# Performance work log

Measured on AMD Instinct MI355X. Metric: run time of the kernel, lower is better.

Reference implementation:

```python
import jax, jax.numpy as jnp
import numpy as np

NEG = -1000000000.0


def setup_inputs() -> dict:
    key = jax.random.key(0)
    ks = jax.random.split(key, 10)
    B, C, D, E, V, G = 512, 200, 512, 256, 8192, 2048  # batch, max_ctx, decoder, embed, vocab, 4*D
    batched_context = jax.random.normal(ks[0], (B, C, D), dtype=jnp.float32)
    counts = jax.random.randint(ks[1], (B,), 1, C + 1, dtype=jnp.int32)
    emb_table = jax.random.normal(ks[2], (V, E), dtype=jnp.float32) * 0.02
    emb_table = emb_table.at[0].set(0.0)  # padding_idx = 0
    W_attn = jax.random.normal(ks[3], (D, D), dtype=jnp.float32) * 0.02
    W_ih = jax.random.normal(ks[4], (G, E + D), dtype=jnp.float32) * 0.02
    b_ih = jax.random.normal(ks[5], (G,), dtype=jnp.float32) * 0.02
    W_hh = jax.random.normal(ks[6], (G, D), dtype=jnp.float32) * 0.02
    b_hh = jax.random.normal(ks[7], (G,), dtype=jnp.float32) * 0.02
    W_proj = jax.random.normal(ks[8], (V, D), dtype=jnp.float32) * 0.02
    b_proj = jax.random.normal(ks[9], (V,), dtype=jnp.float32) * 0.02
    return {
        "batched_context": batched_context, "counts": counts, "output_length": 16,
        "emb_table": emb_table, "W_attn": W_attn, "W_ih": W_ih, "b_ih": b_ih,
        "W_hh": W_hh, "b_hh": b_hh, "W_proj": W_proj, "b_proj": b_proj,
    }


def _decode(batched_context, counts, output_length, emb_table, W_attn, W_ih, b_ih, W_hh, b_hh, W_proj, b_proj):
    B, C, D = batched_context.shape
    V = emb_table.shape[0]
    sos_token = 1
    valid = (jnp.arange(C)[None, :] < counts[:, None])  # [B, C]
    attn_mask = jnp.where(valid, 0.0, NEG).astype(batched_context.dtype)
    # initial state: mean over valid contexts per label
    ctx_masked = batched_context * valid[:, :, None].astype(batched_context.dtype)
    init_state = ctx_masked.sum(axis=1) / counts[:, None].astype(batched_context.dtype)  # [B, D]

    def step(carry, _):
        h, c, tok = carry
        emb = emb_table[tok]  # [B, E]
        # Luong attention on last-layer hidden
        q = h @ W_attn.T  # [B, D]
        score = jnp.einsum("bcd,bd->bc", batched_context, q) + attn_mask
        w = jax.nn.softmax(score, axis=1)  # [B, C]
        context = jnp.einsum("bc,bcd->bd", w, batched_context)  # [B, D]
        x = jnp.concatenate([emb, context], axis=1)  # [B, E+D]
        gates = x @ W_ih.T + b_ih + h @ W_hh.T + b_hh  # [B, 4D]
        i, f, g, o = jnp.split(gates, 4, axis=1)  # PyTorch gate order i,f,g,o
        c_new = jax.nn.sigmoid(f) * c + jax.nn.sigmoid(i) * jnp.tanh(g)
        h_new = jax.nn.sigmoid(o) * jnp.tanh(c_new)
        logits = h_new @ W_proj.T + b_proj  # [B, V]
        tok_new = jnp.argmax(logits, axis=-1)
        return (h_new, c_new, tok_new), logits

    tok0 = jnp.full((B,), sos_token, dtype=jnp.int32)
    _, outs = jax.lax.scan(step, (init_state, init_state, tok0), None, length=output_length - 1)
    zeros0 = jnp.zeros((1, B, V), dtype=batched_context.dtype)  # output[0] stays zero
    return jnp.concatenate([zeros0, outs], axis=0)  # [L, B, V]


def reference(batched_context, counts, output_length, emb_table, W_attn, W_ih, b_ih, W_hh, b_hh, W_proj, b_proj):
    return _decode(batched_context, counts, output_length, emb_table, W_attn, W_ih, b_ih, W_hh, b_hh, W_proj, b_proj)
```

## Files before the change

kernel.cpp:

```cpp
#include <hip/hip_runtime.h>
#include <math.h>

#define B_ 512
#define C_ 200
#define D_ 512
#define E_ 256
#define V_ 8192
#define G_ 2048
#define L_ 16

typedef __attribute__((ext_vector_type(8))) short short8;
typedef __attribute__((ext_vector_type(4))) float f32x4;

__device__ __forceinline__ float sigm(float x) { return 1.0f / (1.0f + expf(-x)); }

__device__ __forceinline__ unsigned short bf16_rn(float x) {
    unsigned int u = __float_as_uint(x);
    return (unsigned short)((u + 0x7FFFu + ((u >> 16) & 1u)) >> 16);
}
__device__ __forceinline__ float bf16f(unsigned short h) {
    return __uint_as_float(((unsigned int)h) << 16);
}


__global__ __launch_bounds__(256) void k_setup(const float* __restrict__ W_proj,
                                               const float* __restrict__ emb,
                                               const float* __restrict__ W_ih,
                                               const float* __restrict__ W_hh,
                                               const float* __restrict__ W_attn,
                                               const float* __restrict__ ctx,
                                               const int* __restrict__ counts,
                                               unsigned short* __restrict__ WpC_hi,
                                               unsigned short* __restrict__ WpC_lo,
                                               unsigned short* __restrict__ Eb_hi,
                                               unsigned short* __restrict__ Eb_lo,
                                               unsigned short* __restrict__ WgC_hi,
                                               unsigned short* __restrict__ WgC_lo,
                                               unsigned short* __restrict__ WaC_hi,
                                               unsigned short* __restrict__ WaC_lo,
                                               unsigned short* __restrict__ h_hi,
                                               unsigned short* __restrict__ h_lo,
                                               float* __restrict__ c,
                                               int* __restrict__ tok) {
    int bb = blockIdx.x;
    int t = threadIdx.x;
    if (bb < 2048) {
        int i = bb * 256 + t;
        int n = i >> 6;
        int koff = (i & 63) * 8;
        float4 v0 = *(const float4*)&W_proj[(size_t)n * 512 + koff];
        float4 v1 = *(const float4*)&W_proj[(size_t)n * 512 + koff + 4];
        float vv[8] = {v0.x, v0.y, v0.z, v0.w, v1.x, v1.y, v1.z, v1.w};
        short8 h8, l8;
#pragma unroll
        for (int e = 0; e < 8; ++e) {
            unsigned short hh = bf16_rn(vv[e]);
            h8[e] = (short)hh;
            l8[e] = (short)bf16_rn(vv[e] - bf16f(hh));
        }
        int nt = n >> 4, srow = n & 15, ktile = koff >> 5, oct = (koff >> 3) & 3;
        size_t off = (((size_t)nt * 16 + ktile) * 64 + (srow + (oct << 4))) * 8;
        *(short8*)&WpC_hi[off] = h8;
        *(short8*)&WpC_lo[off] = l8;
    } else if (bb < 4096) {
        int i = (bb - 2048) * 256 + t;
        float4 v = ((const float4*)emb)[i];
        ushort4 h, l;
        h.x = bf16_rn(v.x); l.x = bf16_rn(v.x - bf16f(h.x));
        h.y = bf16_rn(v.y); l.y = bf16_rn(v.y - bf16f(h.y));
        h.z = bf16_rn(v.z); l.z = bf16_rn(v.z - bf16f(h.z));
        h.w = bf16_rn(v.w); l.w = bf16_rn(v.w - bf16f(h.w));
        ((ushort4*)Eb_hi)[i] = h;
        ((ushort4*)Eb_lo)[i] = l;
    } else if (bb < 5376) {
        int i = (bb - 4096) * 256 + t;
        if (i < 327680) {
            int r = i / 160;
            int koff = (i - r * 160) * 8;
            int go = ((r & 3) << 9) + (r >> 2);
            float4 v0, v1;
            if (koff < 768) {
                v0 = *(const float4*)&W_ih[(size_t)go * 768 + koff];
                v1 = *(const float4*)&W_ih[(size_t)go * 768 + koff + 4];
            } else {
                v0 = *(const float4*)&W_hh[(size_t)go * 512 + (koff - 768)];
                v1 = *(const float4*)&W_hh[(size_t)go * 512 + (koff - 768) + 4];
            }
            float vv[8] = {v0.x, v0.y, v0.z, v0.w, v1.x, v1.y, v1.z, v1.w};
            short8 h8, l8;
#pragma unroll
            for (int e = 0; e < 8; ++e) {
                unsigned short hh = bf16_rn(vv[e]);
                h8[e] = (short)hh;
                l8[e] = (short)bf16_rn(vv[e] - bf16f(hh));
            }
            int nt = r >> 4, srow = r & 15, ktile = koff >> 5, oct = (koff >> 3) & 3;
            size_t off = (((size_t)nt * 40 + ktile) * 64 + (srow + (oct << 4))) * 8;
            *(short8*)&WgC_hi[off] = h8;
            *(short8*)&WgC_lo[off] = l8;
        }
    } else if (bb < 5504) {
        int i = (bb - 5376) * 256 + t;
        int n = i >> 6;
        int koff = (i & 63) * 8;
        float4 v0 = *(const float4*)&W_attn[(size_t)n * 512 + koff];
        float4 v1 = *(const float4*)&W_attn[(size_t)n * 512 + koff + 4];
        float vv[8] = {v0.x, v0.y, v0.z, v0.w, v1.x, v1.y, v1.z, v1.w};
        short8 h8, l8;
#pragma unroll
        for (int e = 0; e < 8; ++e) {
            unsigned short hh = bf16_rn(vv[e]);
            h8[e] = (short)hh;
            l8[e] = (short)bf16_rn(vv[e] - bf16f(hh));
        }
        int nt = n >> 4, srow = n & 15, ktile = koff >> 5, oct = (koff >> 3) & 3;
        size_t off = (((size_t)nt * 16 + ktile) * 64 + (srow + (oct << 4))) * 8;
        *(short8*)&WaC_hi[off] = h8;
        *(short8*)&WaC_lo[off] = l8;
    } else {
        int b = bb - 5504;
        int cnt = counts[b];
        const float* base = ctx + (size_t)b * C_ * D_;
        float s0 = 0.f, s1 = 0.f;
        for (int cc = 0; cc < cnt; ++cc) {
            s0 += base[(size_t)cc * D_ + t];
            s1 += base[(size_t)cc * D_ + t + 256];
        }
        float inv = 1.0f / (float)cnt;
        float v0 = s0 * inv, v1 = s1 * inv;
        c[b * D_ + t] = v0;       c[b * D_ + t + 256] = v1;
        unsigned short p0 = bf16_rn(v0), p1 = bf16_rn(v1);
        h_hi[b * D_ + t] = p0;    h_hi[b * D_ + t + 256] = p1;
        h_lo[b * D_ + t] = bf16_rn(v0 - bf16f(p0));
        h_lo[b * D_ + t + 256] = bf16_rn(v1 - bf16f(p1));
        if (t == 0) tok[b] = 1;
    }
}

template<int PART>
__device__ __forceinline__ void gemm_body(int nb, int mb,
                                          const unsigned short* __restrict__ Ah,
                                          const unsigned short* __restrict__ Al,
                                          const unsigned short* __restrict__ BhC,
                                          const unsigned short* __restrict__ BlC,
                                          const float* __restrict__ bias,
                                          float* __restrict__ C, int ldc,
                                          float* __restrict__ pvO,
                                          int* __restrict__ piO,
                                          short* As,
                                          float (*pvS)[2], int (*piS)[2]) {
    int t = threadIdx.x;
    int l = t & 63;
    int w = t >> 6;
    int m0 = mb * 64;
    int n0 = nb * 128;
    int srow = l & 15;
    int koct = 8 * (l >> 4);
    int pl = w & 1;
    int mtA = w >> 1;
    int wm = w >> 1, wn = w & 1;
    const unsigned short* Apl = pl ? Al : Ah;
    const unsigned short* ApA = Apl + (size_t)(m0 + mtA * 16 + srow) * 512 + koct;
    const unsigned short* ApB = ApA + 32 * 512;
    int ntbase = nb * 8 + wn * 4;
    const unsigned short* Bh0 = BhC + ((size_t)ntbase * 16) * 512 + l * 8;
    const unsigned short* Bl0 = BlC + ((size_t)ntbase * 16) * 512 + l * 8;

    short8 rA0 = *(const short8*)(ApA);
    short8 rA1 = *(const short8*)(ApB);

    f32x4 z = {0.f, 0.f, 0.f, 0.f};
    f32x4 acc[2][4];
#pragma unroll
    for (int i = 0; i < 2; ++i)
#pragma unroll
        for (int j = 0; j < 4; ++j) acc[i][j] = z;

    for (int kt = 0; kt < 16; ++kt) {
        short8 bh[4], bl[4];
#pragma unroll
        for (int j = 0; j < 4; ++j) {
            bh[j] = *(const short8*)(Bh0 + ((size_t)j * 16 + kt) * 512);
            bl[j] = *(const short8*)(Bl0 + ((size_t)j * 16 + kt) * 512);
        }
        __syncthreads();
        *(short8*)&As[(w)*512 + l * 8] = rA0;
        *(short8*)&As[(w + 4) * 512 + l * 8] = rA1;
        __syncthreads();
        if (kt + 1 < 16) {
            int ke = kt * 32;
            rA0 = *(const short8*)(ApA + ke + 32);
            rA1 = *(const short8*)(ApB + ke + 32);
        }
        short8 ah[2], al2[2];
#pragma unroll
        for (int i = 0; i < 2; ++i) {
            ah[i] = *(short8*)&As[((wm * 2 + i) * 2 + 0) * 512 + l * 8];
            al2[i] = *(short8*)&As[((wm * 2 + i) * 2 + 1) * 512 + l * 8];
        }
#pragma unroll
        for (int i = 0; i < 2; ++i)
#pragma unroll
            for (int j = 0; j < 4; ++j) {
                acc[i][j] = __builtin_amdgcn_mfma_f32_16x16x32_bf16(ah[i], bh[j], acc[i][j], 0, 0, 0);
                acc[i][j] = __builtin_amdgcn_mfma_f32_16x16x32_bf16(ah[i], bl[j], acc[i][j], 0, 0, 0);
                acc[i][j] = __builtin_amdgcn_mfma_f32_16x16x32_bf16(al2[i], bh[j], acc[i][j], 0, 0, 0);
            }
    }
    int r0 = (l >> 4) * 4;
    int cl = l & 15;
    if (PART) {
        float bj_[4];
#pragma unroll
        for (int j = 0; j < 4; ++j) bj_[j] = bias[n0 + wn * 64 + j * 16 + cl];
#pragma unroll
        for (int i = 0; i < 2; ++i) {
#pragma unroll
            for (int r = 0; r < 4; ++r) {
                int row = m0 + wm * 32 + i * 16 + r0 + r;
                float bv = -INFINITY;
                int bidx = 0x7fffffff;
#pragma unroll
                for (int j = 0; j < 4; ++j) {
                    int col = n0 + wn * 64 + j * 16 + cl;
                    float v = acc[i][j][r] + bj_[j];
                    C[(size_t)row * ldc + col] = v;
                    if (v > bv) { bv = v; bidx = col; }
                }
#pragma unroll
                for (int off = 1; off < 16; off <<= 1) {
                    float ov = __shfl_xor(bv, off);
                    int oi = __shfl_xor(bidx, off);
                    if (ov > bv || (ov == bv && oi < bidx)) { bv = ov; bidx = oi; }
                }
                if (cl == 0) {
                    pvS[wm * 32 + i * 16 + r0 + r][wn] = bv;
                    piS[wm * 32 + i * 16 + r0 + r][wn] = bidx;
                }
            }
        }
        __syncthreads();
        if (t < 64) {
            float v0 = pvS[t][0], v1 = pvS[t][1];
            int i0 = piS[t][0], i1 = piS[t][1];
            bool take1 = (v1 > v0);
            pvO[(size_t)(m0 + t) * 64 + nb] = take1 ? v1 : v0;
            piO[(size_t)(m0 + t) * 64 + nb] = take1 ? i1 : i0;
        }
    } else {
#pragma unroll
        for (int i = 0; i < 2; ++i)
#pragma unroll
            for (int j = 0; j < 4; ++j) {
                int col = n0 + wn * 64 + j * 16 + cl;
                int rowb = m0 + wm * 32 + i * 16 + r0;
#pragma unroll
                for (int r = 0; r < 4; ++r)
                    C[(size_t)(rowb + r) * ldc + col] = acc[i][j][r];
            }
    }
}

__global__ __launch_bounds__(256, 2) void k_mega(const unsigned short* __restrict__ Ah,
                                                 const unsigned short* __restrict__ Al,
                                                 const unsigned short* __restrict__ WpCh,
                                                 const unsigned short* __restrict__ WpCl,
                                                 const float* __restrict__ bias,
                                                 float* __restrict__ Cl_,
                                                 float* __restrict__ pvO,
                                                 int* __restrict__ piO,
                                                 const unsigned short* __restrict__ WaCh,
                                                 const unsigned short* __restrict__ WaCl,
                                                 float* __restrict__ qbuf) {
    __shared__ short As[8 * 512];
    __shared__ float pvS[64][2];
    __shared__ int piS[64][2];
    int bb = blockIdx.x;
    if (bb < 512) {
        int xcd = bb & 7, lid = bb >> 3;
        int nb = xcd * 8 + (lid & 7);
        int mb = lid >> 3;
        gemm_body<1>(nb, mb, Ah, Al, WpCh, WpCl, bias, Cl_, V_, pvO, piO,
                     As, pvS, piS);
    } else {
        int idx = bb - 512;
        int nb = idx & 3, mb = idx >> 2;
        gemm_body<0>(nb, mb, Ah, Al, WaCh, WaCl, nullptr, qbuf, D_, nullptr, nullptr,
                     As, pvS, piS);
    }
}

__global__ __launch_bounds__(256, 2) void k_qproj(const unsigned short* __restrict__ Ah,
                                                  const unsigned short* __restrict__ Al,
                                                  const unsigned short* __restrict__ WaCh,
                                                  const unsigned short* __restrict__ WaCl,
                                                  float* __restrict__ qbuf) {
    __shared__ short As[8 * 512];
    __shared__ float pvS[64][2];
    __shared__ int piS[64][2];
    int nb = blockIdx.x & 3, mb = blockIdx.x >> 2;
    gemm_body<0>(nb, mb, Ah, Al, WaCh, WaCl, nullptr, qbuf, D_, nullptr, nullptr,
                 As, pvS, piS);
}

__global__ __launch_bounds__(256) void k_attn(const float* __restrict__ ctx,
                                              const int* __restrict__ counts,
                                              const float* __restrict__ q,
                                              unsigned short* __restrict__ cv_hi,
                                              unsigned short* __restrict__ cv_lo) {
    __shared__ float accw[4][512];
    __shared__ float mw_s[4], sw_s[4];
    int b = blockIdx.x;
    int t = threadIdx.x;
    int lane = t & 63;
    int wv = t >> 6;
    int cnt = counts[b];
    const float* cb = ctx + (size_t)b * C_ * D_;

    float4 q0 = *(const float4*)&q[(size_t)b * D_ + lane * 4];
    float4 q1 = *(const float4*)&q[(size_t)b * D_ + lane * 4 + 256];

    float m_w = -INFINITY, s_w = 0.f;
    float4 a0 = make_float4(0.f, 0.f, 0.f, 0.f);
    float4 a1 = make_float4(0.f, 0.f, 0.f, 0.f);

#define ATT_DOT(x0, x1) (x0.x * q0.x + x0.y * q0.y + x0.z * q0.z + x0.w * q0.w + \
                         x1.x * q1.x + x1.y * q1.y + x1.z * q1.z + x1.w * q1.w)
#define ATT_UPD(s, x0, x1)                                                     \
    {                                                                          \
        float e;                                                               \
        if (s > m_w) {                                                         \
            float sc = expf(m_w - s);                                          \
            s_w = s_w * sc + 1.f;                                              \
            a0.x *= sc; a0.y *= sc; a0.z *= sc; a0.w *= sc;                    \
            a1.x *= sc; a1.y *= sc; a1.z *= sc; a1.w *= sc;                    \
            m_w = s; e = 1.f;                                                  \
        } else {                                                               \
            e = expf(s - m_w);                                                 \
            s_w += e;                                                          \
        }                                                                      \
        a0.x += e * x0.x; a0.y += e * x0.y; a0.z += e * x0.z; a0.w += e * x0.w;\
        a1.x += e * x1.x; a1.y += e * x1.y; a1.z += e * x1.z; a1.w += e * x1.w;\
    }

    int cc = wv;
    for (; cc + 4 < cnt; cc += 8) {
        const float* rA = cb + (size_t)cc * D_;
        const float* rB = cb + (size_t)(cc + 4) * D_;
        float4 xa0 = *(const float4*)&rA[lane * 4];
        float4 xa1 = *(const float4*)&rA[lane * 4 + 256];
        float4 xb0 = *(const float4*)&rB[lane * 4];
        float4 xb1 = *(const float4*)&rB[lane * 4 + 256];
        float sa = ATT_DOT(xa0, xa1);
        float sb = ATT_DOT(xb0, xb1);
#pragma unroll
        for (int off = 32; off; off >>= 1) {
            sa += __shfl_xor(sa, off);
            sb += __shfl_xor(sb, off);
        }
        ATT_UPD(sa, xa0, xa1);
        ATT_UPD(sb, xb0, xb1);
    }
    if (cc < cnt) {
        const float* rA = cb + (size_t)cc * D_;
        float4 xa0 = *(const float4*)&rA[lane * 4];
        float4 xa1 = *(const float4*)&rA[lane * 4 + 256];
        float sa = ATT_DOT(xa0, xa1);
#pragma unroll
        for (int off = 32; off; off >>= 1) sa += __shfl_xor(sa, off);
        ATT_UPD(sa, xa0, xa1);
    }

    accw[wv][lane * 4 + 0] = a0.x; accw[wv][lane * 4 + 1] = a0.y;
    accw[wv][lane * 4 + 2] = a0.z; accw[wv][lane * 4 + 3] = a0.w;
    accw[wv][256 + lane * 4 + 0] = a1.x; accw[wv][256 + lane * 4 + 1] = a1.y;
    accw[wv][256 + lane * 4 + 2] = a1.z; accw[wv][256 + lane * 4 + 3] = a1.w;
    if (lane == 0) { mw_s[wv] = m_w; sw_s[wv] = s_w; }
    __syncthreads();

    float m_g = fmaxf(fmaxf(mw_s[0], mw_s[1]), fmaxf(mw_s[2], mw_s[3]));
    float e0 = expf(mw_s[0] - m_g), e1 = expf(mw_s[1] - m_g);
    float e2 = expf(mw_s[2] - m_g), e3 = expf(mw_s[3] - m_g);
    float inv = 1.0f / (sw_s[0] * e0 + sw_s[1] * e1 + sw_s[2] * e2 + sw_s[3] * e3);
    float v0 = (accw[0][t] * e0 + accw[1][t] * e1 + accw[2][t] * e2 + accw[3][t] * e3) * inv;
    float v1 = (accw[0][t + 256] * e0 + accw[1][t + 256] * e1 +
                accw[2][t + 256] * e2 + accw[3][t + 256] * e3) * inv;
    unsigned short p0 = bf16_rn(v0), p1 = bf16_rn(v1);
    cv_hi[(size_t)b * D_ + t] = p0;
    cv_hi[(size_t)b * D_ + t + 256] = p1;
    cv_lo[(size_t)b * D_ + t] = bf16_rn(v0 - bf16f(p0));
    cv_lo[(size_t)b * D_ + t + 256] = bf16_rn(v1 - bf16f(p1));
}

template<int RED>
__global__ __launch_bounds__(256, 2) void k_gatesm(const int* __restrict__ tok,
                                                   const float* __restrict__ pvO,
                                                   const int* __restrict__ piO,
                                                   const unsigned short* __restrict__ Eh,
                                                   const unsigned short* __restrict__ El,
                                                   const unsigned short* __restrict__ Ch,
                                                   const unsigned short* __restrict__ Cl,
                                                   const unsigned short* __restrict__ Hh,
                                                   const unsigned short* __restrict__ Hl,
                                                   const unsigned short* __restrict__ WgCh,
                                                   const unsigned short* __restrict__ WgCl,
                                                   const float* __restrict__ b_ih,
                                                   const float* __restrict__ b_hh,
                                                   float* __restrict__ cbuf,
                                                   unsigned short* __restrict__ Hoh,
                                                   unsigned short* __restrict__ Hol) {
    __shared__ short As[8 * 512];
    __shared__ int toks[64];
    int bid = blockIdx.x;
    int t = threadIdx.x;
    int l = t & 63;
    int w = t >> 6;
    int xcd = bid & 7, lid = bid >> 3;
    int nb = xcd * 8 + (lid & 7);
    int mb = lid >> 3;
    int m0 = mb * 64;
    int n0 = nb * 32;
    int srow = l & 15;
    int koct = 8 * (l >> 4);
    int pl = w & 1;
    int mtA = w >> 1;
    int locA = mtA * 16 + srow;
    int rowA = m0 + locA;
    int rowB = rowA + 32;

    if (RED) {
        int ri = t >> 2, qq = t & 3;
        const float* pv = pvO + (size_t)(m0 + ri) * 64 + qq * 16;
        const int* pi = piO + (size_t)(m0 + ri) * 64 + qq * 16;
        float bv = -INFINITY;
        int bix = 0x7fffffff;
#pragma unroll
        for (int j = 0; j < 16; ++j) {
            float v = pv[j];
            int ii = pi[j];
            if (v > bv || (v == bv && ii < bix)) { bv = v; bix = ii; }
        }
#pragma unroll
        for (int off = 1; off < 4; off <<= 1) {
            float ov = __shfl_xor(bv, off);
            int oi = __shfl_xor(bix, off);
            if (ov > bv || (ov == bv && oi < bix)) { bv = ov; bix = oi; }
        }
        if (qq == 0) toks[ri] = bix;
        __syncthreads();
    }

    int tokA = RED ? toks[locA] : tok[rowA];
    int tokB = RED ? toks[locA + 32] : tok[rowB];

    const unsigned short* Ep = pl ? El : Eh;
    const unsigned short* Cp = pl ? Cl : Ch;
    const unsigned short* Hp = pl ? Hl : Hh;
    int wm = w >> 1, wn = w & 1;
    int ntg = nb * 2 + wn;
    const unsigned short* Bh0 = WgCh + ((size_t)ntg * 40) * 512 + l * 8;
    const unsigned short* Bl0 = WgCl + ((size_t)ntg * 40) * 512 + l * 8;

    f32x4 z = {0.f, 0.f, 0.f, 0.f};
    f32x4 acc[2];
    acc[0] = z; acc[1] = z;

    short8 rA0, rA1;

#define GATES_LOADA(dst, row, tk, kk)                                          \
    {                                                                          \
        int kx = (kk);                                                         \
        if (kx < 256)      dst = *(const short8*)&Ep[(size_t)(tk)*256 + kx];   \
        else if (kx < 768) dst = *(const short8*)&Cp[(size_t)(row)*512 + (kx - 256)]; \
        else               dst = *(const short8*)&Hp[(size_t)(row)*512 + (kx - 768)]; \
    }

    GATES_LOADA(rA0, rowA, tokA, koct);
    GATES_LOADA(rA1, rowB, tokB, koct);

    for (int kt = 0; kt < 40; ++kt) {
        short8 bh = *(const short8*)(Bh0 + (size_t)kt * 512);
        short8 bl = *(const short8*)(Bl0 + (size_t)kt * 512);
        __syncthreads();
        *(short8*)&As[(w)*512 + l * 8] = rA0;
        *(short8*)&As[(w + 4) * 512 + l * 8] = rA1;
        __syncthreads();
        if (kt + 1 < 40) {
            int ke = kt * 32;
            GATES_LOADA(rA0, rowA, tokA, ke + 32 + koct);
            GATES_LOADA(rA1, rowB, tokB, ke + 32 + koct);
        }
        short8 ah[2], al2[2];
#pragma unroll
        for (int i = 0; i < 2; ++i) {
            ah[i] = *(short8*)&As[((wm * 2 + i) * 2 + 0) * 512 + l * 8];
            al2[i] = *(short8*)&As[((wm * 2 + i) * 2 + 1) * 512 + l * 8];
        }
#pragma unroll
        for (int i = 0; i < 2; ++i) {
            acc[i] = __builtin_amdgcn_mfma_f32_16x16x32_bf16(ah[i], bh, acc[i], 0, 0, 0);
            acc[i] = __builtin_amdgcn_mfma_f32_16x16x32_bf16(ah[i], bl, acc[i], 0, 0, 0);
            acc[i] = __builtin_amdgcn_mfma_f32_16x16x32_bf16(al2[i], bh, acc[i], 0, 0, 0);
        }
    }

    int r0 = (l >> 4) * 4;
    int cl = l & 15;
    bool act = (cl & 3) == 0;
    int gc = n0 + wn * 16 + cl;
    int d = gc >> 2;
    float bi_ = b_ih[d] + b_hh[d];
    float bf_ = b_ih[512 + d] + b_hh[512 + d];
    float bg_ = b_ih[1024 + d] + b_hh[1024 + d];
    float bo_ = b_ih[1536 + d] + b_hh[1536 + d];
#pragma unroll
    for (int i = 0; i < 2; ++i) {
#pragma unroll
        for (int r = 0; r < 4; ++r) {
            float x = acc[i][r];
            float x1 = __shfl_xor(x, 1);
            float x2 = __shfl_xor(x, 2);
            float x3 = __shfl_xor(x, 3);
            if (act) {
                int row = m0 + wm * 32 + i * 16 + r0 + r;
                float ig = sigm(x + bi_);
                float fg = sigm(x1 + bf_);
                float gg = tanhf(x2 + bg_);
                float og = sigm(x3 + bo_);
                float cn = fg * cbuf[(size_t)row * D_ + d] + ig * gg;
                cbuf[(size_t)row * D_ + d] = cn;
                float hv = og * tanhf(cn);
                unsigned short hh = bf16_rn(hv);
                Hoh[(size_t)row * D_ + d] = hh;
                Hol[(size_t)row * D_ + d] = bf16_rn(hv - bf16f(hh));
            }
        }
    }
}

extern "C" void kernel_launch(void* const* d_in, const int* in_sizes, int n_in,
                              void* d_out, int out_size, void* d_ws, size_t ws_size,
                              hipStream_t stream) {
    const float* ctx    = (const float*)d_in[0];
    const int*   counts = (const int*)d_in[1];
    const float* emb    = (const float*)d_in[3];
    const float* W_attn = (const float*)d_in[4];
    const float* W_ih   = (const float*)d_in[5];
    const float* b_ih   = (const float*)d_in[6];
    const float* W_hh   = (const float*)d_in[7];
    const float* b_hh   = (const float*)d_in[8];
    const float* W_proj = (const float*)d_in[9];
    const float* b_proj = (const float*)d_in[10];
    float* out = (float*)d_out;

    float* qbuf = (float*)d_ws;
    float* cbuf = qbuf + B_ * D_;
    unsigned short* p = (unsigned short*)(cbuf + B_ * D_);
    unsigned short* Wa_hi = p; p += D_ * D_;
    unsigned short* Wa_lo = p; p += D_ * D_;
    unsigned short* Wp_hi = p; p += (size_t)V_ * D_;
    unsigned short* Wp_lo = p; p += (size_t)V_ * D_;
    unsigned short* Eb_hi = p; p += (size_t)V_ * E_;
    unsigned short* Eb_lo = p; p += (size_t)V_ * E_;
    unsigned short* Wg_hi = p; p += (size_t)G_ * 1280;
    unsigned short* Wg_lo = p; p += (size_t)G_ * 1280;
    unsigned short* hA_hi = p; p += B_ * D_;
    unsigned short* hA_lo = p; p += B_ * D_;
    unsigned short* hB_hi = p; p += B_ * D_;
    unsigned short* hB_lo = p; p += B_ * D_;
    unsigned short* cv_hi = p; p += B_ * D_;
    unsigned short* cv_lo = p; p += B_ * D_;
    int* tok = (int*)p;
    float* pvO = (float*)(tok + B_);
    int* piO = (int*)(pvO + B_ * 64);

    k_setup<<<6016, 256, 0, stream>>>(W_proj, emb, W_ih, W_hh, W_attn, ctx, counts,
                                      Wp_hi, Wp_lo, Eb_hi, Eb_lo, Wg_hi, Wg_lo,
                                      Wa_hi, Wa_lo, hA_hi, hA_lo, cbuf, tok);

    hipMemsetAsync(out, 0, (size_t)B_ * V_ * sizeof(float), stream);

    k_qproj<<<32, 256, 0, stream>>>(hA_hi, hA_lo, Wa_hi, Wa_lo, qbuf);

    unsigned short *hin_hi = hA_hi, *hin_lo = hA_lo;
    unsigned short *hout_hi = hB_hi, *hout_lo = hB_lo;
    for (int t = 1; t < L_; ++t) {
        k_attn<<<B_, 256, 0, stream>>>(ctx, counts, qbuf, cv_hi, cv_lo);
        if (t == 1) {
            k_gatesm<0><<<512, 256, 0, stream>>>(
                tok, pvO, piO, Eb_hi, Eb_lo, cv_hi, cv_lo, hin_hi, hin_lo,
                Wg_hi, Wg_lo, b_ih, b_hh, cbuf, hout_hi, hout_lo);
        } else {
            k_gatesm<1><<<512, 256, 0, stream>>>(
                tok, pvO, piO, Eb_hi, Eb_lo, cv_hi, cv_lo, hin_hi, hin_lo,
                Wg_hi, Wg_lo, b_ih, b_hh, cbuf, hout_hi, hout_lo);
        }
        float* slab = out + (size_t)t * B_ * V_;
        k_mega<<<544, 256, 0, stream>>>(hout_hi, hout_lo, Wp_hi, Wp_lo, b_proj,
                                        slab, pvO, piO, Wa_hi, Wa_lo, qbuf);
        unsigned short* tmp;
        tmp = hin_hi; hin_hi = hout_hi; hout_hi = tmp;
        tmp = hin_lo; hin_lo = hout_lo; hout_lo = tmp;
    }
}
```

Before: 1.480 ms.

## Store activations in MFMA-fragment layout and drop LDS staging in GEMMs

Hidden state, context vector and initial h are now written in the same tiled fragment layout as the weights, so the GEMM kernels can load A operands straight from global memory into registers. This removes the shared-memory staging and the two __syncthreads per k-step in gemm_body and the gates kernel. The gates kernel's K loop is split into three loops (embedding, context, hidden), which removes per-iteration branching. Separately, the output slab zeroing is folded into the setup kernel in place of a memset launch. The cost is more redundant global/L2 loads of A, since each wave now fetches its own A rows instead of sharing them through LDS.

```diff
diff --git a/kernel.cpp b/kernel.cpp
--- a/kernel.cpp
+++ b/kernel.cpp
@@ -22,6 +22,10 @@
     return __uint_as_float(((unsigned int)h) << 16);
 }
 
+__device__ __forceinline__ size_t canon_off(int row, int k, int NKT) {
+    return ((((size_t)(row >> 4) * NKT + (k >> 5)) * 64) +
+            ((row & 15) + (((k >> 3) & 3) << 4))) * 8 + (k & 7);
+}
 
 __global__ __launch_bounds__(256) void k_setup(const float* __restrict__ W_proj,
                                                const float* __restrict__ emb,
@@ -41,7 +45,8 @@
                                                unsigned short* __restrict__ h_hi,
                                                unsigned short* __restrict__ h_lo,
                                                float* __restrict__ c,
-                                               int* __restrict__ tok) {
+                                               int* __restrict__ tok,
+                                               float* __restrict__ out0) {
     int bb = blockIdx.x;
     int t = threadIdx.x;
     if (bb < 2048) {
@@ -58,8 +63,7 @@
             h8[e] = (short)hh;
             l8[e] = (short)bf16_rn(vv[e] - bf16f(hh));
         }
-        int nt = n >> 4, srow = n & 15, ktile = koff >> 5, oct = (koff >> 3) & 3;
-        size_t off = (((size_t)nt * 16 + ktile) * 64 + (srow + (oct << 4))) * 8;
+        size_t off = canon_off(n, koff, 16);
         *(short8*)&WpC_hi[off] = h8;
         *(short8*)&WpC_lo[off] = l8;
     } else if (bb < 4096) {
@@ -94,8 +98,7 @@
                 h8[e] = (short)hh;
                 l8[e] = (short)bf16_rn(vv[e] - bf16f(hh));
             }
-            int nt = r >> 4, srow = r & 15, ktile = koff >> 5, oct = (koff >> 3) & 3;
-            size_t off = (((size_t)nt * 40 + ktile) * 64 + (srow + (oct << 4))) * 8;
+            size_t off = canon_off(r, koff, 40);
             *(short8*)&WgC_hi[off] = h8;
             *(short8*)&WgC_lo[off] = l8;
         }
@@ -113,11 +116,10 @@
             h8[e] = (short)hh;
             l8[e] = (short)bf16_rn(vv[e] - bf16f(hh));
         }
-        int nt = n >> 4, srow = n & 15, ktile = koff >> 5, oct = (koff >> 3) & 3;
-        size_t off = (((size_t)nt * 16 + ktile) * 64 + (srow + (oct << 4))) * 8;
+        size_t off = canon_off(n, koff, 16);
         *(short8*)&WaC_hi[off] = h8;
         *(short8*)&WaC_lo[off] = l8;
-    } else {
+    } else if (bb < 6016) {
         int b = bb - 5504;
         int cnt = counts[b];
         const float* base = ctx + (size_t)b * C_ * D_;
@@ -130,10 +132,15 @@
         float v0 = s0 * inv, v1 = s1 * inv;
         c[b * D_ + t] = v0;       c[b * D_ + t + 256] = v1;
         unsigned short p0 = bf16_rn(v0), p1 = bf16_rn(v1);
-        h_hi[b * D_ + t] = p0;    h_hi[b * D_ + t + 256] = p1;
-        h_lo[b * D_ + t] = bf16_rn(v0 - bf16f(p0));
-        h_lo[b * D_ + t + 256] = bf16_rn(v1 - bf16f(p1));
+        size_t o0 = canon_off(b, t, 16);
+        size_t o1 = canon_off(b, t + 256, 16);
+        h_hi[o0] = p0;            h_hi[o1] = p1;
+        h_lo[o0] = bf16_rn(v0 - bf16f(p0));
+        h_lo[o1] = bf16_rn(v1 - bf16f(p1));
         if (t == 0) tok[b] = 1;
+    } else {
+        int i = (bb - 6016) * 256 + t;
+        ((float4*)out0)[i] = make_float4(0.f, 0.f, 0.f, 0.f);
     }
 }
 
@@ -147,28 +154,20 @@
                                           float* __restrict__ C, int ldc,
                                           float* __restrict__ pvO,
                                           int* __restrict__ piO,
-                                          short* As,
                                           float (*pvS)[2], int (*piS)[2]) {
     int t = threadIdx.x;
     int l = t & 63;
     int w = t >> 6;
+    int wm = w >> 1, wn = w & 1;
     int m0 = mb * 64;
     int n0 = nb * 128;
-    int srow = l & 15;
-    int koct = 8 * (l >> 4);
-    int pl = w & 1;
-    int mtA = w >> 1;
-    int wm = w >> 1, wn = w & 1;
-    const unsigned short* Apl = pl ? Al : Ah;
-    const unsigned short* ApA = Apl + (size_t)(m0 + mtA * 16 + srow) * 512 + koct;
-    const unsigned short* ApB = ApA + 32 * 512;
+    int tA0 = mb * 4 + wm * 2;
+    const unsigned short* Ah0 = Ah + ((size_t)tA0 * 16) * 512 + l * 8;
+    const unsigned short* Al0 = Al + ((size_t)tA0 * 16) * 512 + l * 8;
     int ntbase = nb * 8 + wn * 4;
     const unsigned short* Bh0 = BhC + ((size_t)ntbase * 16) * 512 + l * 8;
     const unsigned short* Bl0 = BlC + ((size_t)ntbase * 16) * 512 + l * 8;
 
-    short8 rA0 = *(const short8*)(ApA);
-    short8 rA1 = *(const short8*)(ApB);
-
     f32x4 z = {0.f, 0.f, 0.f, 0.f};
     f32x4 acc[2][4];
 #pragma unroll
@@ -177,26 +176,18 @@
         for (int j = 0; j < 4; ++j) acc[i][j] = z;
 
     for (int kt = 0; kt < 16; ++kt) {
-        short8 bh[4], bl[4];
+        short8 ah[2], al[2], bh[4], bl[4];
+#pragma unroll
+        for (int i = 0; i < 2; ++i) {
+            size_t o = ((size_t)i * 16 + kt) * 512;
+            ah[i] = *(const short8*)(Ah0 + o);
+            al[i] = *(const short8*)(Al0 + o);
+        }
 #pragma unroll
         for (int j = 0; j < 4; ++j) {
-            bh[j] = *(const short8*)(Bh0 + ((size_t)j * 16 + kt) * 512);
-            bl[j] = *(const short8*)(Bl0 + ((size_t)j * 16 + kt) * 512);
-        }
-        __syncthreads();
-        *(short8*)&As[(w)*512 + l * 8] = rA0;
-        *(short8*)&As[(w + 4) * 512 + l * 8] = rA1;
-        __syncthreads();
-        if (kt + 1 < 16) {
-            int ke = kt * 32;
-            rA0 = *(const short8*)(ApA + ke + 32);
-            rA1 = *(const short8*)(ApB + ke + 32);
-        }
-        short8 ah[2], al2[2];
-#pragma unroll
-        for (int i = 0; i < 2; ++i) {
-            ah[i] = *(short8*)&As[((wm * 2 + i) * 2 + 0) * 512 + l * 8];
-            al2[i] = *(short8*)&As[((wm * 2 + i) * 2 + 1) * 512 + l * 8];
+            size_t o = ((size_t)j * 16 + kt) * 512;
+            bh[j] = *(const short8*)(Bh0 + o);
+            bl[j] = *(const short8*)(Bl0 + o);
         }
 #pragma unroll
         for (int i = 0; i < 2; ++i)
@@ -204,7 +195,7 @@
             for (int j = 0; j < 4; ++j) {
                 acc[i][j] = __builtin_amdgcn_mfma_f32_16x16x32_bf16(ah[i], bh[j], acc[i][j], 0, 0, 0);
                 acc[i][j] = __builtin_amdgcn_mfma_f32_16x16x32_bf16(ah[i], bl[j], acc[i][j], 0, 0, 0);
-                acc[i][j] = __builtin_amdgcn_mfma_f32_16x16x32_bf16(al2[i], bh[j], acc[i][j], 0, 0, 0);
+                acc[i][j] = __builtin_amdgcn_mfma_f32_16x16x32_bf16(al[i], bh[j], acc[i][j], 0, 0, 0);
             }
     }
     int r0 = (l >> 4) * 4;
@@ -272,7 +263,6 @@
                                                  const unsigned short* __restrict__ WaCh,
                                                  const unsigned short* __restrict__ WaCl,
                                                  float* __restrict__ qbuf) {
-    __shared__ short As[8 * 512];
     __shared__ float pvS[64][2];
     __shared__ int piS[64][2];
     int bb = blockIdx.x;
@@ -280,13 +270,11 @@
         int xcd = bb & 7, lid = bb >> 3;
         int nb = xcd * 8 + (lid & 7);
         int mb = lid >> 3;
-        gemm_body<1>(nb, mb, Ah, Al, WpCh, WpCl, bias, Cl_, V_, pvO, piO,
-                     As, pvS, piS);
+        gemm_body<1>(nb, mb, Ah, Al, WpCh, WpCl, bias, Cl_, V_, pvO, piO, pvS, piS);
     } else {
         int idx = bb - 512;
         int nb = idx & 3, mb = idx >> 2;
-        gemm_body<0>(nb, mb, Ah, Al, WaCh, WaCl, nullptr, qbuf, D_, nullptr, nullptr,
-                     As, pvS, piS);
+        gemm_body<0>(nb, mb, Ah, Al, WaCh, WaCl, nullptr, qbuf, D_, nullptr, nullptr, pvS, piS);
     }
 }
 
@@ -295,12 +283,10 @@
                                                   const unsigned short* __restrict__ WaCh,
                                                   const unsigned short* __restrict__ WaCl,
                                                   float* __restrict__ qbuf) {
-    __shared__ short As[8 * 512];
     __shared__ float pvS[64][2];
     __shared__ int piS[64][2];
     int nb = blockIdx.x & 3, mb = blockIdx.x >> 2;
-    gemm_body<0>(nb, mb, Ah, Al, WaCh, WaCl, nullptr, qbuf, D_, nullptr, nullptr,
-                 As, pvS, piS);
+    gemm_body<0>(nb, mb, Ah, Al, WaCh, WaCl, nullptr, qbuf, D_, nullptr, nullptr, pvS, piS);
 }
 
 __global__ __launch_bounds__(256) void k_attn(const float* __restrict__ ctx,
@@ -386,10 +372,12 @@
     float v1 = (accw[0][t + 256] * e0 + accw[1][t + 256] * e1 +
                 accw[2][t + 256] * e2 + accw[3][t + 256] * e3) * inv;
     unsigned short p0 = bf16_rn(v0), p1 = bf16_rn(v1);
-    cv_hi[(size_t)b * D_ + t] = p0;
-    cv_hi[(size_t)b * D_ + t + 256] = p1;
-    cv_lo[(size_t)b * D_ + t] = bf16_rn(v0 - bf16f(p0));
-    cv_lo[(size_t)b * D_ + t + 256] = bf16_rn(v1 - bf16f(p1));
+    size_t o0 = canon_off(b, t, 16);
+    size_t o1 = canon_off(b, t + 256, 16);
+    cv_hi[o0] = p0;
+    cv_hi[o1] = p1;
+    cv_lo[o0] = bf16_rn(v0 - bf16f(p0));
+    cv_lo[o1] = bf16_rn(v1 - bf16f(p1));
 }
 
 template<int RED>
@@ -409,24 +397,18 @@
                                                    float* __restrict__ cbuf,
                                                    unsigned short* __restrict__ Hoh,
                                                    unsigned short* __restrict__ Hol) {
-    __shared__ short As[8 * 512];
     __shared__ int toks[64];
     int bid = blockIdx.x;
     int t = threadIdx.x;
     int l = t & 63;
     int w = t >> 6;
+    int wm = w >> 1, wn = w & 1;
     int xcd = bid & 7, lid = bid >> 3;
     int nb = xcd * 8 + (lid & 7);
     int mb = lid >> 3;
     int m0 = mb * 64;
     int n0 = nb * 32;
-    int srow = l & 15;
     int koct = 8 * (l >> 4);
-    int pl = w & 1;
-    int mtA = w >> 1;
-    int locA = mtA * 16 + srow;
-    int rowA = m0 + locA;
-    int rowB = rowA + 32;
 
     if (RED) {
         int ri = t >> 2, qq = t & 3;
@@ -450,13 +432,14 @@
         __syncthreads();
     }
 
-    int tokA = RED ? toks[locA] : tok[rowA];
-    int tokB = RED ? toks[locA + 32] : tok[rowB];
-
-    const unsigned short* Ep = pl ? El : Eh;
-    const unsigned short* Cp = pl ? Cl : Ch;
-    const unsigned short* Hp = pl ? Hl : Hh;
-    int wm = w >> 1, wn = w & 1;
+    int lr0 = wm * 32 + (l & 15);
+    int tk0 = RED ? toks[lr0] : tok[m0 + lr0];
+    int tk1 = RED ? toks[lr0 + 16] : tok[m0 + lr0 + 16];
+    int tg0 = mb * 4 + wm * 2;
+    const unsigned short* Ch0 = Ch + ((size_t)tg0 * 16) * 512 + l * 8;
+    const unsigned short* Cl0 = Cl + ((size_t)tg0 * 16) * 512 + l * 8;
+    const unsigned short* Hh0 = Hh + ((size_t)tg0 * 16) * 512 + l * 8;
+    const unsigned short* Hl0 = Hl + ((size_t)tg0 * 16) * 512 + l * 8;
     int ntg = nb * 2 + wn;
     const unsigned short* Bh0 = WgCh + ((size_t)ntg * 40) * 512 + l * 8;
     const unsigned short* Bl0 = WgCl + ((size_t)ntg * 40) * 512 + l * 8;
@@ -465,43 +448,43 @@
     f32x4 acc[2];
     acc[0] = z; acc[1] = z;
 
-    short8 rA0, rA1;
-
-#define GATES_LOADA(dst, row, tk, kk)                                          \
-    {                                                                          \
-        int kx = (kk);                                                         \
-        if (kx < 256)      dst = *(const short8*)&Ep[(size_t)(tk)*256 + kx];   \
-        else if (kx < 768) dst = *(const short8*)&Cp[(size_t)(row)*512 + (kx - 256)]; \
-        else               dst = *(const short8*)&Hp[(size_t)(row)*512 + (kx - 768)]; \
-    }
-
-    GATES_LOADA(rA0, rowA, tokA, koct);
-    GATES_LOADA(rA1, rowB, tokB, koct);
-
-    for (int kt = 0; kt < 40; ++kt) {
+#define GATES_MFMA(a0h, a0l, a1h, a1l, bh, bl)                                   \
+    acc[0] = __builtin_amdgcn_mfma_f32_16x16x32_bf16(a0h, bh, acc[0], 0, 0, 0);  \
+    acc[0] = __builtin_amdgcn_mfma_f32_16x16x32_bf16(a0h, bl, acc[0], 0, 0, 0);  \
+    acc[0] = __builtin_amdgcn_mfma_f32_16x16x32_bf16(a0l, bh, acc[0], 0, 0, 0);  \
+    acc[1] = __builtin_amdgcn_mfma_f32_16x16x32_bf16(a1h, bh, acc[1], 0, 0, 0);  \
+    acc[1] = __builtin_amdgcn_mfma_f32_16x16x32_bf16(a1h, bl, acc[1], 0, 0, 0);  \
+    acc[1] = __builtin_amdgcn_mfma_f32_16x16x32_bf16(a1l, bh, acc[1], 0, 0, 0);
+
+    for (int kt = 0; kt < 8; ++kt) {
+        int ko = kt * 32 + koct;
+        short8 a0h = *(const short8*)&Eh[(size_t)tk0 * 256 + ko];
+        short8 a0l = *(const short8*)&El[(size_t)tk0 * 256 + ko];
+        short8 a1h = *(const short8*)&Eh[(size_t)tk1 * 256 + ko];
+        short8 a1l = *(const short8*)&El[(size_t)tk1 * 256 + ko];
         short8 bh = *(const short8*)(Bh0 + (size_t)kt * 512);
         short8 bl = *(const short8*)(Bl0 + (size_t)kt * 512);
-        __syncthreads();
-        *(short8*)&As[(w)*512 + l * 8] = rA0;
-        *(short8*)&As[(w + 4) * 512 + l * 8] = rA1;
-        __syncthreads();
-        if (kt + 1 < 40) {
-            int ke = kt * 32;
-            GATES_LOADA(rA0, rowA, tokA, ke + 32 + koct);
-            GATES_LOADA(rA1, rowB, tokB, ke + 32 + koct);
-        }
-        short8 ah[2], al2[2];
-#pragma unroll
-        for (int i = 0; i < 2; ++i) {
-            ah[i] = *(short8*)&As[((wm * 2 + i) * 2 + 0) * 512 + l * 8];
-            al2[i] = *(short8*)&As[((wm * 2 + i) * 2 + 1) * 512 + l * 8];
-        }
-#pragma unroll
-        for (int i = 0; i < 2; ++i) {
-            acc[i] = __builtin_amdgcn_mfma_f32_16x16x32_bf16(ah[i], bh, acc[i], 0, 0, 0);
-            acc[i] = __builtin_amdgcn_mfma_f32_16x16x32_bf16(ah[i], bl, acc[i], 0, 0, 0);
-            acc[i] = __builtin_amdgcn_mfma_f32_16x16x32_bf16(al2[i], bh, acc[i], 0, 0, 0);
-        }
+        GATES_MFMA(a0h, a0l, a1h, a1l, bh, bl)
+    }
+    for (int kt = 8; kt < 24; ++kt) {
+        size_t oc = ((size_t)(kt - 8)) * 512;
+        short8 a0h = *(const short8*)(Ch0 + oc);
+        short8 a0l = *(const short8*)(Cl0 + oc);
+        short8 a1h = *(const short8*)(Ch0 + 16 * 512 + oc);
+        short8 a1l = *(const short8*)(Cl0 + 16 * 512 + oc);
+        short8 bh = *(const short8*)(Bh0 + (size_t)kt * 512);
+        short8 bl = *(const short8*)(Bl0 + (size_t)kt * 512);
+        GATES_MFMA(a0h, a0l, a1h, a1l, bh, bl)
+    }
+    for (int kt = 24; kt < 40; ++kt) {
+        size_t oh = ((size_t)(kt - 24)) * 512;
+        short8 a0h = *(const short8*)(Hh0 + oh);
+        short8 a0l = *(const short8*)(Hl0 + oh);
+        short8 a1h = *(const short8*)(Hh0 + 16 * 512 + oh);
+        short8 a1l = *(const short8*)(Hl0 + 16 * 512 + oh);
+        short8 bh = *(const short8*)(Bh0 + (size_t)kt * 512);
+        short8 bl = *(const short8*)(Bl0 + (size_t)kt * 512);
+        GATES_MFMA(a0h, a0l, a1h, a1l, bh, bl)
     }
 
     int r0 = (l >> 4) * 4;
@@ -531,8 +514,9 @@
                 cbuf[(size_t)row * D_ + d] = cn;
                 float hv = og * tanhf(cn);
                 unsigned short hh = bf16_rn(hv);
-                Hoh[(size_t)row * D_ + d] = hh;
-                Hol[(size_t)row * D_ + d] = bf16_rn(hv - bf16f(hh));
+                size_t oo = canon_off(row, d, 16);
+                Hoh[oo] = hh;
+                Hol[oo] = bf16_rn(hv - bf16f(hh));
             }
         }
     }
@@ -574,11 +558,9 @@
     float* pvO = (float*)(tok + B_);
     int* piO = (int*)(pvO + B_ * 64);
 
-    k_setup<<<6016, 256, 0, stream>>>(W_proj, emb, W_ih, W_hh, W_attn, ctx, counts,
-                                      Wp_hi, Wp_lo, Eb_hi, Eb_lo, Wg_hi, Wg_lo,
-                                      Wa_hi, Wa_lo, hA_hi, hA_lo, cbuf, tok);
-
-    hipMemsetAsync(out, 0, (size_t)B_ * V_ * sizeof(float), stream);
+    k_setup<<<10112, 256, 0, stream>>>(W_proj, emb, W_ih, W_hh, W_attn, ctx, counts,
+                                       Wp_hi, Wp_lo, Eb_hi, Eb_lo, Wg_hi, Wg_lo,
+                                       Wa_hi, Wa_lo, hA_hi, hA_lo, cbuf, tok, out);
 
     k_qproj<<<32, 256, 0, stream>>>(hA_hi, hA_lo, Wa_hi, Wa_lo, qbuf);
 
```

Measured after the change: 1.463 ms. About the same (-1.2%).
